# Kernel optimization log

Hardware: AMD Instinct MI355X
Metric: run time of the kernel (lower is better)

## Reference

```python
import jax, jax.numpy as jnp
import numpy as np


def setup_inputs() -> dict:
    key = jax.random.key(0)
    k1, k2 = jax.random.split(key)
    x = jax.random.normal(k1, (16, 256, 4096), dtype=jnp.float32)          # [B, D, T]
    codebooks = jax.random.normal(k2, (8, 1024, 256), dtype=jnp.float32)   # [n_q, bins, D]
    return {"x": x, "codebooks": codebooks}


def _quantize_one(residual, embed):
    """residual: [B, T, D]; embed: [bins, D] -> (quantize [B,T,D], idx [B,T])."""
    # negative squared euclidean distance (encodec euclidean codebook)
    x_sq = jnp.sum(residual * residual, axis=-1, keepdims=True)            # [B, T, 1]
    e_sq = jnp.sum(embed * embed, axis=-1)                                  # [bins]
    dots = jnp.einsum("btd,nd->btn", residual, embed)                       # [B, T, bins]
    dist = -(x_sq - 2.0 * dots + e_sq)                                      # [B, T, bins]
    idx = jnp.argmax(dist, axis=-1)                                         # [B, T] int
    quantize = embed[idx]                                                   # gather [B, T, D]
    return quantize, idx


def reference(x, codebooks):
    """Residual VQ forward (inference path, EMA updates omitted).
    x: [B, D, T]; codebooks: [n_q, bins, D].
    Returns (quantized [B, D, T], codes [n_q, B, T]).
    """
    n_q = codebooks.shape[0]
    residual = jnp.transpose(x, (0, 2, 1))                                  # [B, T, D]
    quantized_out = jnp.zeros_like(residual)
    codes = []
    for q in range(n_q):  # small fixed structural loop over quantizer stages
        quantize, idx = _quantize_one(residual, codebooks[q])
        # straight-through estimator as in encodec VectorQuantization
        quantize = residual + jax.lax.stop_gradient(quantize - residual)
        residual = residual - quantize
        quantized_out = quantized_out + quantize
        codes.append(idx)
    quantized = jnp.transpose(quantized_out, (0, 2, 1))                     # [B, D, T]
    codes = jnp.stack(codes, axis=0)                                        # [n_q, B, T]
    return quantized, codes
```

## Files before the change

### kernel.cpp

```cpp
#include <hip/hip_runtime.h>


#define BB   16
#define DD   256
#define TT   4096
#define NQ   8
#define BINS 1024
#define DELTA 4.0f
#define SOFF  8192.0f
#define OUTQ ((size_t)BB * DD * TT)

typedef _Float16 half8 __attribute__((ext_vector_type(8)));
typedef float    facc  __attribute__((ext_vector_type(4)));

#define MFMA16(A, B, C) __builtin_amdgcn_mfma_f32_16x16x32_f16((A), (B), (C), 0, 0, 0)

__global__ __launch_bounds__(256)
void rvq_pack_h16(const float* __restrict__ cb, _Float16* __restrict__ pks) {
    int gid = blockIdx.x * 256 + threadIdx.x;
    int s   = gid & 7;
    int bin = (gid >> 3) & 1023;
    int q   = gid >> 13;
    const float* src = cb + ((size_t)(q * BINS + bin)) * DD + s * 32;
    int cc    = q * 32 + (bin >> 5);
    int nf    = (bin >> 4) & 1;
    int c     = bin & 15;
    int plane = nf * 8 + s;
    size_t base = (size_t)cc * 8192 + (size_t)plane * 512 + c * 8;
    #pragma unroll
    for (int g = 0; g < 4; ++g) {
        float4 v0 = *(const float4*)(src + g * 8);
        float4 v1 = *(const float4*)(src + g * 8 + 4);
        float vv[8] = { v0.x, v0.y, v0.z, v0.w, v1.x, v1.y, v1.z, v1.w };
        half8 h8;
        #pragma unroll
        for (int j = 0; j < 8; ++j) h8[j] = (_Float16)vv[j];
        *(half8*)&pks[base + g * 128] = h8;
    }
}

__global__ __launch_bounds__(256)
void rvq_esq_off(const float* __restrict__ cb, float* __restrict__ hoff) {
    int q = blockIdx.x;
    const float* e = cb + (size_t)q * BINS * DD;
    for (int bin = threadIdx.x; bin < BINS; bin += 256) {
        const float4* row = (const float4*)(e + (size_t)bin * DD);
        float s = 0.f;
        #pragma unroll 8
        for (int i = 0; i < DD / 4; ++i) {
            float4 v = row[i];
            s += v.x * v.x + v.y * v.y + v.z * v.z + v.w * v.w;
        }
        hoff[q * BINS + bin] = SOFF - 8.0f * s;
    }
}

__global__ __launch_bounds__(128, 2)
void rvq_mfma8_kernel(const float* __restrict__ x, const float* __restrict__ cb,
                      const _Float16* __restrict__ pks, const float* __restrict__ hoff,
                      float* __restrict__ out)
{
    __shared__ alignas(16) _Float16 btile[2][16][512];
    __shared__ float esq_lds[BINS];
    __shared__ unsigned short best_lds[2][32];
    __shared__ unsigned short hist_lds[2][NQ][32];

    const int tid = threadIdx.x;
    const int w   = tid >> 6;
    const int l   = tid & 63;
    const int c   = l & 15;
    const int g   = l >> 4;

    const int blk = blockIdx.x;
    const int b   = blk >> 6;
    const int t0  = (blk & 63) * 64;
    const int tw  = t0 + w * 32;

    const char* gsrc0 = (const char*)pks + w * 8192 + (l << 4);

    auto issue_chunk = [&](int k, int bu) {
        k &= 255;
        const char* src = gsrc0 + (size_t)k * 16384;
        char* dst = (char*)(&btile[bu][0][0]) + w * 8192;
        #pragma unroll
        for (int i = 0; i < 8; ++i) {
            __builtin_amdgcn_global_load_lds(
                (const __attribute__((address_space(1))) unsigned int*)(src + i * 1024),
                (__attribute__((address_space(3))) unsigned int*)(dst + i * 1024),
                16, 0, 0);
        }
    };

    issue_chunk(0, 0);

    half8 rh[2][8], rl[2][8];
    {
        const float* xb = x + (size_t)b * DD * TT;
        #pragma unroll
        for (int s = 0; s < 8; ++s) {
            #pragma unroll
            for (int j = 0; j < 8; ++j) {
                int d = s * 32 + g * 8 + j;
                #pragma unroll
                for (int m = 0; m < 2; ++m) {
                    int t = tw + m * 16 + c;
                    float v = 16.0f * xb[(size_t)d * TT + t];
                    _Float16 h = (_Float16)v;
                    rh[m][s][j] = h;
                    rl[m][s][j] = (_Float16)(v - (float)h);
                }
            }
        }
    }
    {
        float4 v0 = *(const float4*)(hoff + tid * 8);
        float4 v1 = *(const float4*)(hoff + tid * 8 + 4);
        *(float4*)&esq_lds[tid * 8]     = v0;
        *(float4*)&esq_lds[tid * 8 + 4] = v1;
    }
    __syncthreads();

    float p1[2][4], p2[2][4], p3[2][4];

    auto reset_slots = [&]() {
        #pragma unroll
        for (int m = 0; m < 2; ++m)
            #pragma unroll
            for (int j = 0; j < 4; ++j) { p1[m][j] = 0.f; p2[m][j] = 0.f; p3[m][j] = 0.f; }
    };

    auto compute_chunk = [&](int bu, int ch) {
        facc a00 = {0.f,0.f,0.f,0.f}, a01 = {0.f,0.f,0.f,0.f};
        facc a10 = {0.f,0.f,0.f,0.f}, a11 = {0.f,0.f,0.f,0.f};
        const int roff = g * 128 + c * 8;
        const float q0 = esq_lds[ch * 32 + c];
        const float q1 = esq_lds[ch * 32 + 16 + c];
        const _Float16 (*bt)[512] = btile[bu];

        __builtin_amdgcn_s_setprio(1);
        #pragma unroll
        for (int s = 0; s < 8; ++s) {
            half8 b0 = *(const half8*)&bt[s][roff];
            half8 b1 = *(const half8*)&bt[8 + s][roff];
            a00 = MFMA16(rh[0][s], b0, a00);
            a10 = MFMA16(rh[1][s], b0, a10);
            a01 = MFMA16(rh[0][s], b1, a01);
            a11 = MFMA16(rh[1][s], b1, a11);
        }
        __builtin_amdgcn_s_setprio(0);

        const unsigned idx0 = 1023u - (unsigned)(ch * 32 + c);
        const unsigned idx1 = idx0 - 16u;
        #pragma unroll
        for (int fm = 0; fm < 2; ++fm) {
            #pragma unroll
            for (int fj = 0; fj < 4; ++fj) {
                float s0 = (fm ? a10[fj] : a00[fj]) + q0;
                float s1 = (fm ? a11[fj] : a01[fj]) + q1;
                float v0 = __builtin_bit_cast(float,
                             (__builtin_bit_cast(unsigned, s0) & ~1023u) | idx0);
                float v1 = __builtin_bit_cast(float,
                             (__builtin_bit_cast(unsigned, s1) & ~1023u) | idx1);
                float h1 = fmaxf(p1[fm][fj], v0), l1 = fminf(p1[fm][fj], v0);
                float h2 = fmaxf(p2[fm][fj], l1), l2 = fminf(p2[fm][fj], l1);
                p1[fm][fj] = h1; p2[fm][fj] = h2; p3[fm][fj] = fmaxf(p3[fm][fj], l2);
                h1 = fmaxf(p1[fm][fj], v1); l1 = fminf(p1[fm][fj], v1);
                h2 = fmaxf(p2[fm][fj], l1); l2 = fminf(p2[fm][fj], l1);
                p1[fm][fj] = h1; p2[fm][fj] = h2; p3[fm][fj] = fmaxf(p3[fm][fj], l2);
            }
        }
    };

    auto refine3 = [&](int tkl, int qq, int c1, int c2, int c3) -> int {
        int t = tw + tkl;
        double pa = 0.0, pb = 0.0, pc = 0.0;
        const float* e1p = cb + (size_t)(qq * BINS + c1) * DD;
        const float* e2p = cb + (size_t)(qq * BINS + c2) * DD;
        const float* e3p = cb + (size_t)(qq * BINS + c3) * DD;
        #pragma unroll
        for (int dd = 0; dd < 4; ++dd) {
            int d = l * 4 + dd;
            float rv = x[((size_t)b * DD + d) * TT + t];
            for (int k = 0; k < qq; ++k) {
                int hb = hist_lds[w][k][tkl];
                rv -= cb[(size_t)(k * BINS + hb) * DD + d];
            }
            float e1v = e1p[d], e2v = e2p[d], e3v = e3p[d];
            pa += (double)e1v * (2.0 * (double)rv - (double)e1v);
            pb += (double)e2v * (2.0 * (double)rv - (double)e2v);
            pc += (double)e3v * (2.0 * (double)rv - (double)e3v);
        }
        #pragma unroll
        for (int mk = 1; mk < 64; mk <<= 1) {
            pa += __shfl_xor(pa, mk);
            pb += __shfl_xor(pb, mk);
            pc += __shfl_xor(pc, mk);
        }
        int wbin = c1; double pw = pa;
        if (pb > pw || (pb == pw && c2 < wbin)) { pw = pb; wbin = c2; }
        if (pc > pw || (pc == pw && c3 < wbin)) { pw = pc; wbin = c3; }
        return wbin;
    };

    auto stage_end = [&](int qq) {
        int  bch[2][4], cn2[2][4], cn3[2][4];
        bool gate[2][4];
        #pragma unroll
        for (int fm = 0; fm < 2; ++fm) {
            #pragma unroll
            for (int fj = 0; fj < 4; ++fj) {
                float a1 = p1[fm][fj], a2 = p2[fm][fj], a3 = p3[fm][fj];
                #pragma unroll
                for (int mk = 1; mk < 16; mk <<= 1) {
                    float b1 = __shfl_xor(a1, mk);
                    float b2 = __shfl_xor(a2, mk);
                    float b3 = __shfl_xor(a3, mk);
                    float lo1 = fminf(a1, b1);
                    float m22 = fmaxf(a2, b2);
                    float r1  = fmaxf(a1, b1);
                    float r2  = fmaxf(lo1, m22);
                    float r3  = fmaxf(fminf(lo1, m22), fmaxf(fminf(a2, b2), fmaxf(a3, b3)));
                    a1 = r1; a2 = r2; a3 = r3;
                }
                bch[fm][fj] = 1023 - (int)(__builtin_bit_cast(unsigned, a1) & 1023u);
                cn2[fm][fj] = 1023 - (int)(__builtin_bit_cast(unsigned, a2) & 1023u);
                cn3[fm][fj] = 1023 - (int)(__builtin_bit_cast(unsigned, a3) & 1023u);
                gate[fm][fj] = (a1 - a2 <= DELTA);
            }
        }
        bool anyg = gate[0][0] | gate[0][1] | gate[0][2] | gate[0][3]
                  | gate[1][0] | gate[1][1] | gate[1][2] | gate[1][3];
        if (__any(anyg)) {
            #pragma unroll
            for (int fm = 0; fm < 2; ++fm) {
                #pragma unroll
                for (int fj = 0; fj < 4; ++fj) {
                    unsigned long long nm = __ballot(gate[fm][fj]);
                    if (nm) {
                        for (int g2 = 0; g2 < 4; ++g2) {
                            if ((nm >> (g2 * 16)) & 1ull) {
                                int c1 = __shfl(bch[fm][fj], g2 * 16);
                                int c2 = __shfl(cn2[fm][fj], g2 * 16);
                                int c3 = __shfl(cn3[fm][fj], g2 * 16);
                                int tkl = fm * 16 + g2 * 4 + fj;
                                int wb = refine3(tkl, qq, c1, c2, c3);
                                if (g == g2) bch[fm][fj] = wb;
                            }
                        }
                    }
                }
            }
        }

        if (c == 0) {
            #pragma unroll
            for (int fm = 0; fm < 2; ++fm)
                #pragma unroll
                for (int fj = 0; fj < 4; ++fj) {
                    int tkl = fm * 16 + g * 4 + fj;
                    best_lds[w][tkl] = (unsigned short)bch[fm][fj];
                    hist_lds[w][qq][tkl] = (unsigned short)bch[fm][fj];
                    out[OUTQ + ((size_t)qq * BB + b) * TT + tw + tkl] = (float)bch[fm][fj];
                }
        }

        #pragma unroll
        for (int m = 0; m < 2; ++m) {
            int bin = best_lds[w][m * 16 + c];
            const float* ep = cb + (size_t)(qq * BINS + bin) * DD + g * 8;
            #pragma unroll
            for (int s = 0; s < 8; ++s) {
                float4 e0 = *(const float4*)(ep + s * 32);
                float4 e1 = *(const float4*)(ep + s * 32 + 4);
                float ev[8] = { e0.x, e0.y, e0.z, e0.w, e1.x, e1.y, e1.z, e1.w };
                #pragma unroll
                for (int j = 0; j < 8; ++j) {
                    float rv = (float)rh[m][s][j] + (float)rl[m][s][j];
                    float nr = rv - 16.0f * ev[j];
                    _Float16 nh = (_Float16)nr;
                    rh[m][s][j] = nh;
                    rl[m][s][j] = (_Float16)(nr - (float)nh);
                }
            }
        }
    };

    int buf = 0;
    #pragma unroll 1
    for (int q = 0; q < NQ; ++q) {
        reset_slots();
        #pragma unroll 1
        for (int ch = 0; ch < 32; ++ch) {
            issue_chunk(q * 32 + ch + 1, buf ^ 1);
            compute_chunk(buf, ch);
            if (ch == 31) stage_end(q);
            __syncthreads();
            buf ^= 1;
        }
        if (q + 1 < NQ) {
            float4 v0 = *(const float4*)(hoff + (q + 1) * BINS + tid * 8);
            float4 v1 = *(const float4*)(hoff + (q + 1) * BINS + tid * 8 + 4);
            *(float4*)&esq_lds[tid * 8]     = v0;
            *(float4*)&esq_lds[tid * 8 + 4] = v1;
            __syncthreads();
        }
    }

    {
        const float* xb = x + (size_t)b * DD * TT;
        float* ob = out + (size_t)b * DD * TT;
        #pragma unroll
        for (int s = 0; s < 8; ++s)
            #pragma unroll
            for (int j = 0; j < 8; ++j) {
                int d = s * 32 + g * 8 + j;
                #pragma unroll
                for (int m = 0; m < 2; ++m) {
                    int t = tw + m * 16 + c;
                    float rv = ((float)rh[m][s][j] + (float)rl[m][s][j]) * 0.0625f;
                    ob[(size_t)d * TT + t] = xb[(size_t)d * TT + t] - rv;
                }
            }
    }
}

#define TOK_PER_BLK 32
#define BIN_CHUNK   128
#define KC          32
#define EPAD        36
#define RPAD        260
#define FDELTA      0.0078125f

#define FUPD2(S, BIN, B1, I1, B2, I2)                                        \
    if ((S) > (B2) || ((S) == (B2) && (BIN) < (I2))) {                      \
        if ((S) > (B1) || ((S) == (B1) && (BIN) < (I1))) {                  \
            B2 = B1; I2 = I1; B1 = (S); I1 = (BIN);                         \
        } else { B2 = (S); I2 = (BIN); }                                    \
    }

__global__ __launch_bounds__(256, 2)
void rvq_esq_kernel(const float* __restrict__ cb, float* __restrict__ esq) {
    int q = blockIdx.x;
    const float* e = cb + (size_t)q * BINS * DD;
    for (int bin = threadIdx.x; bin < BINS; bin += 256) {
        const float4* row = (const float4*)(e + (size_t)bin * DD);
        float s = 0.f;
        #pragma unroll 8
        for (int i = 0; i < DD / 4; ++i) {
            float4 v = row[i];
            s += v.x * v.x + v.y * v.y + v.z * v.z + v.w * v.w;
        }
        esq[q * BINS + bin] = s;
    }
}

__global__ __launch_bounds__(256, 2)
void rvq_main_kernel(const float* __restrict__ x, const float* __restrict__ cb,
                     const float* __restrict__ esq, float* __restrict__ out) {
    __shared__ float r_lds[TOK_PER_BLK][RPAD];
    __shared__ float e_lds[BIN_CHUNK][EPAD];
    __shared__ float red_s[16][2][TOK_PER_BLK];
    __shared__ int   red_i[16][2][TOK_PER_BLK];
    __shared__ int   best_lds2[TOK_PER_BLK];

    const int tid = threadIdx.x;
    const int blk = blockIdx.x;
    const int b   = blk >> 7;
    const int t0  = (blk & 127) * TOK_PER_BLK;

    {
        const int tl = tid & 31;
        const int d0 = (tid >> 5) * 32;
        const float* xp = x + (size_t)b * DD * TT + t0 + tl;
        for (int dd = 0; dd < 32; ++dd) {
            int d = d0 + dd;
            r_lds[tl][d] = xp[(size_t)d * TT];
        }
    }
    __syncthreads();

    const int ty = tid >> 4;
    const int tx = tid & 15;

    for (int q = 0; q < NQ; ++q) {
        const float* eb = cb + (size_t)q * BINS * DD;
        const float* es = esq + q * BINS;
        float b1[2] = {-1e30f, -1e30f}, b2[2] = {-1e30f, -1e30f};
        int   i1[2] = {0x7fffffff, 0x7fffffff}, i2[2] = {0x7fffffff, 0x7fffffff};

        for (int cch = 0; cch < BINS / BIN_CHUNK; ++cch) {
            float acc[2][8];
            #pragma unroll
            for (int i = 0; i < 2; ++i)
                #pragma unroll
                for (int j = 0; j < 8; ++j) acc[i][j] = 0.f;

            for (int kc = 0; kc < DD / KC; ++kc) {
                __syncthreads();
                {
                    const int col  = tid & 7;
                    const int row0 = tid >> 3;
                    const float* src = eb + (size_t)(cch * BIN_CHUNK) * DD + kc * KC;
                    #pragma unroll
                    for (int rr = 0; rr < 4; ++rr) {
                        int row = row0 + rr * 32;
                        float4 v = *(const float4*)(src + (size_t)row * DD + col * 4);
                        *(float4*)&e_lds[row][col * 4] = v;
                    }
                }
                __syncthreads();
                #pragma unroll
                for (int k4 = 0; k4 < KC / 4; ++k4) {
                    float4 r0 = *(const float4*)&r_lds[tx][kc * KC + k4 * 4];
                    float4 r1 = *(const float4*)&r_lds[tx + 16][kc * KC + k4 * 4];
                    #pragma unroll
                    for (int bi = 0; bi < 8; ++bi) {
                        float4 e4 = *(const float4*)&e_lds[ty + 16 * bi][k4 * 4];
                        acc[0][bi] += r0.x * e4.x + r0.y * e4.y + r0.z * e4.z + r0.w * e4.w;
                        acc[1][bi] += r1.x * e4.x + r1.y * e4.y + r1.z * e4.z + r1.w * e4.w;
                    }
                }
            }
            #pragma unroll
            for (int bi = 0; bi < 8; ++bi) {
                int bin = cch * BIN_CHUNK + ty + 16 * bi;
                float half_esq = 0.5f * es[bin];
                float s0 = acc[0][bi] - half_esq;
                float s1v = acc[1][bi] - half_esq;
                FUPD2(s0, bin, b1[0], i1[0], b2[0], i2[0]);
                FUPD2(s1v, bin, b1[1], i1[1], b2[1], i2[1]);
            }
        }

        #pragma unroll
        for (int k = 0; k < 2; ++k) {
            red_s[ty][k][tx]      = k ? b2[0] : b1[0];
            red_i[ty][k][tx]      = k ? i2[0] : i1[0];
            red_s[ty][k][tx + 16] = k ? b2[1] : b1[1];
            red_i[ty][k][tx + 16] = k ? i2[1] : i1[1];
        }
        __syncthreads();

        if (tid < TOK_PER_BLK) {
            float g1 = -1e30f, g2 = -1e30f; int gi1 = 0x7fffffff, gi2 = 0x7fffffff;
            #pragma unroll
            for (int j = 0; j < 16; ++j) {
                #pragma unroll
                for (int k = 0; k < 2; ++k) {
                    float s = red_s[j][k][tid]; int ii = red_i[j][k][tid];
                    FUPD2(s, ii, g1, gi1, g2, gi2);
                }
            }
            int bif;
            if (g1 - g2 <= FDELTA) {
                const float* rrow = r_lds[tid];
                double sc[2]; int id2[2] = { gi1, gi2 };
                for (int cc2 = 0; cc2 < 2; ++cc2) {
                    const float* ep = eb + (size_t)id2[cc2] * DD;
                    double acc2 = 0.0;
                    #pragma unroll 4
                    for (int d = 0; d < DD; ++d) {
                        double ev = (double)ep[d];
                        acc2 += ev * (2.0 * (double)rrow[d] - ev);
                    }
                    sc[cc2] = acc2;
                }
                bif = (sc[0] > sc[1] || (sc[0] == sc[1] && id2[0] < id2[1])) ? id2[0] : id2[1];
            } else {
                bif = gi1;
            }
            best_lds2[tid] = bif;
            out[OUTQ + (size_t)q * (BB * TT) + (size_t)b * TT + t0 + tid] = (float)bif;
        }
        __syncthreads();

        {
            const int tok  = tid >> 3;
            const int part = tid & 7;
            const int bin  = best_lds2[tok];
            const float* ep = eb + (size_t)bin * DD + part * 32;
            float* rp = &r_lds[tok][part * 32];
            #pragma unroll
            for (int dd = 0; dd < 32; ++dd) rp[dd] -= ep[dd];
        }
        __syncthreads();
    }

    {
        const int tl = tid & 31;
        const int d0 = (tid >> 5) * 32;
        const float* xp = x + (size_t)b * DD * TT + t0 + tl;
        float*       op = out + (size_t)b * DD * TT + t0 + tl;
        for (int dd = 0; dd < 32; ++dd) {
            int d = d0 + dd;
            op[(size_t)d * TT] = xp[(size_t)d * TT] - r_lds[tl][d];
        }
    }
}

extern "C" void kernel_launch(void* const* d_in, const int* in_sizes, int n_in,
                              void* d_out, int out_size, void* d_ws, size_t ws_size,
                              hipStream_t stream) {
    const float* x  = (const float*)d_in[0];
    const float* cb = (const float*)d_in[1];
    float* out = (float*)d_out;

    const size_t PKS_BYTES = (size_t)NQ * BINS * DD * 2;
    const size_t NEED = PKS_BYTES + (size_t)NQ * BINS * 4;

    if (ws_size >= NEED) {
        _Float16* pks = (_Float16*)d_ws;
        float* hoff = (float*)((char*)d_ws + PKS_BYTES);
        rvq_pack_h16<<<(NQ * BINS * 8) / 256, 256, 0, stream>>>(cb, pks);
        rvq_esq_off<<<NQ, 256, 0, stream>>>(cb, hoff);
        rvq_mfma8_kernel<<<1024, 128, 0, stream>>>(x, cb, pks, hoff, out);
    } else {
        float* esq = (float*)d_ws;
        rvq_esq_kernel<<<NQ, 256, 0, stream>>>(cb, esq);
        rvq_main_kernel<<<(BB * TT) / TOK_PER_BLK, 256, 0, stream>>>(x, cb, esq, out);
    }
}
```

Baseline: 658.9 us.

## Split each block's 64 tokens across four waves of 16 tokens

Blocks grow from 2 waves owning 32 tokens each to 4 waves owning 16 tokens each. Each wave now keeps a single 16-row MFMA tile, which halves the per-wave residual and accumulator registers, and the LDS codebook chunk loads are shared across 4 waves. The intent is higher occupancy and more waves to hide latency. In exchange, each loaded B fragment now feeds 2 MFMAs per wave instead of 4, so LDS read traffic per FLOP doubles and block-level syncs cover more waves.

Result: faster. 635.0 us (-3.6%).

```diff
diff --git a/kernel.cpp b/kernel.cpp
--- a/kernel.cpp
+++ b/kernel.cpp
@@ -55,15 +55,15 @@
     }
 }
 
-__global__ __launch_bounds__(128, 2)
-void rvq_mfma8_kernel(const float* __restrict__ x, const float* __restrict__ cb,
+__global__ __launch_bounds__(256, 4)
+void rvq_mfma9_kernel(const float* __restrict__ x, const float* __restrict__ cb,
                       const _Float16* __restrict__ pks, const float* __restrict__ hoff,
                       float* __restrict__ out)
 {
     __shared__ alignas(16) _Float16 btile[2][16][512];
     __shared__ float esq_lds[BINS];
-    __shared__ unsigned short best_lds[2][32];
-    __shared__ unsigned short hist_lds[2][NQ][32];
+    __shared__ unsigned short best_lds[4][16];
+    __shared__ unsigned short hist_lds[4][NQ][16];
 
     const int tid = threadIdx.x;
     const int w   = tid >> 6;
@@ -74,16 +74,16 @@
     const int blk = blockIdx.x;
     const int b   = blk >> 6;
     const int t0  = (blk & 63) * 64;
-    const int tw  = t0 + w * 32;
-
-    const char* gsrc0 = (const char*)pks + w * 8192 + (l << 4);
+    const int tw  = t0 + w * 16;
+
+    const char* gsrc0 = (const char*)pks + w * 4096 + (l << 4);
 
     auto issue_chunk = [&](int k, int bu) {
         k &= 255;
         const char* src = gsrc0 + (size_t)k * 16384;
-        char* dst = (char*)(&btile[bu][0][0]) + w * 8192;
-        #pragma unroll
-        for (int i = 0; i < 8; ++i) {
+        char* dst = (char*)(&btile[bu][0][0]) + w * 4096;
+        #pragma unroll
+        for (int i = 0; i < 4; ++i) {
             __builtin_amdgcn_global_load_lds(
                 (const __attribute__((address_space(1))) unsigned int*)(src + i * 1024),
                 (__attribute__((address_space(3))) unsigned int*)(dst + i * 1024),
@@ -93,45 +93,37 @@
 
     issue_chunk(0, 0);
 
-    half8 rh[2][8], rl[2][8];
+    half8 rh[8], rl[8];
     {
         const float* xb = x + (size_t)b * DD * TT;
+        const int t = tw + c;
         #pragma unroll
         for (int s = 0; s < 8; ++s) {
             #pragma unroll
             for (int j = 0; j < 8; ++j) {
                 int d = s * 32 + g * 8 + j;
-                #pragma unroll
-                for (int m = 0; m < 2; ++m) {
-                    int t = tw + m * 16 + c;
-                    float v = 16.0f * xb[(size_t)d * TT + t];
-                    _Float16 h = (_Float16)v;
-                    rh[m][s][j] = h;
-                    rl[m][s][j] = (_Float16)(v - (float)h);
-                }
+                float v = 16.0f * xb[(size_t)d * TT + t];
+                _Float16 h = (_Float16)v;
+                rh[s][j] = h;
+                rl[s][j] = (_Float16)(v - (float)h);
             }
         }
     }
     {
-        float4 v0 = *(const float4*)(hoff + tid * 8);
-        float4 v1 = *(const float4*)(hoff + tid * 8 + 4);
-        *(float4*)&esq_lds[tid * 8]     = v0;
-        *(float4*)&esq_lds[tid * 8 + 4] = v1;
+        float4 v = *(const float4*)(hoff + tid * 4);
+        *(float4*)&esq_lds[tid * 4] = v;
     }
     __syncthreads();
 
-    float p1[2][4], p2[2][4], p3[2][4];
+    float p1[4], p2[4], p3[4];
 
     auto reset_slots = [&]() {
         #pragma unroll
-        for (int m = 0; m < 2; ++m)
-            #pragma unroll
-            for (int j = 0; j < 4; ++j) { p1[m][j] = 0.f; p2[m][j] = 0.f; p3[m][j] = 0.f; }
+        for (int j = 0; j < 4; ++j) { p1[j] = 0.f; p2[j] = 0.f; p3[j] = 0.f; }
     };
 
     auto compute_chunk = [&](int bu, int ch) {
-        facc a00 = {0.f,0.f,0.f,0.f}, a01 = {0.f,0.f,0.f,0.f};
-        facc a10 = {0.f,0.f,0.f,0.f}, a11 = {0.f,0.f,0.f,0.f};
+        facc a0 = {0.f,0.f,0.f,0.f}, a1 = {0.f,0.f,0.f,0.f};
         const int roff = g * 128 + c * 8;
         const float q0 = esq_lds[ch * 32 + c];
         const float q1 = esq_lds[ch * 32 + 16 + c];
@@ -142,32 +134,27 @@
         for (int s = 0; s < 8; ++s) {
             half8 b0 = *(const half8*)&bt[s][roff];
             half8 b1 = *(const half8*)&bt[8 + s][roff];
-            a00 = MFMA16(rh[0][s], b0, a00);
-            a10 = MFMA16(rh[1][s], b0, a10);
-            a01 = MFMA16(rh[0][s], b1, a01);
-            a11 = MFMA16(rh[1][s], b1, a11);
+            a0 = MFMA16(rh[s], b0, a0);
+            a1 = MFMA16(rh[s], b1, a1);
         }
         __builtin_amdgcn_s_setprio(0);
 
         const unsigned idx0 = 1023u - (unsigned)(ch * 32 + c);
         const unsigned idx1 = idx0 - 16u;
         #pragma unroll
-        for (int fm = 0; fm < 2; ++fm) {
-            #pragma unroll
-            for (int fj = 0; fj < 4; ++fj) {
-                float s0 = (fm ? a10[fj] : a00[fj]) + q0;
-                float s1 = (fm ? a11[fj] : a01[fj]) + q1;
-                float v0 = __builtin_bit_cast(float,
-                             (__builtin_bit_cast(unsigned, s0) & ~1023u) | idx0);
-                float v1 = __builtin_bit_cast(float,
-                             (__builtin_bit_cast(unsigned, s1) & ~1023u) | idx1);
-                float h1 = fmaxf(p1[fm][fj], v0), l1 = fminf(p1[fm][fj], v0);
-                float h2 = fmaxf(p2[fm][fj], l1), l2 = fminf(p2[fm][fj], l1);
-                p1[fm][fj] = h1; p2[fm][fj] = h2; p3[fm][fj] = fmaxf(p3[fm][fj], l2);
-                h1 = fmaxf(p1[fm][fj], v1); l1 = fminf(p1[fm][fj], v1);
-                h2 = fmaxf(p2[fm][fj], l1); l2 = fminf(p2[fm][fj], l1);
-                p1[fm][fj] = h1; p2[fm][fj] = h2; p3[fm][fj] = fmaxf(p3[fm][fj], l2);
-            }
+        for (int fj = 0; fj < 4; ++fj) {
+            float s0 = a0[fj] + q0;
+            float s1 = a1[fj] + q1;
+            float v0 = __builtin_bit_cast(float,
+                         (__builtin_bit_cast(unsigned, s0) & ~1023u) | idx0);
+            float v1 = __builtin_bit_cast(float,
+                         (__builtin_bit_cast(unsigned, s1) & ~1023u) | idx1);
+            float h1 = fmaxf(p1[fj], v0), l1 = fminf(p1[fj], v0);
+            float h2 = fmaxf(p2[fj], l1), l2 = fminf(p2[fj], l1);
+            p1[fj] = h1; p2[fj] = h2; p3[fj] = fmaxf(p3[fj], l2);
+            h1 = fmaxf(p1[fj], v1); l1 = fminf(p1[fj], v1);
+            h2 = fmaxf(p2[fj], l1); l2 = fminf(p2[fj], l1);
+            p1[fj] = h1; p2[fj] = h2; p3[fj] = fmaxf(p3[fj], l2);
         }
     };
 
@@ -203,49 +190,42 @@
     };
 
     auto stage_end = [&](int qq) {
-        int  bch[2][4], cn2[2][4], cn3[2][4];
-        bool gate[2][4];
-        #pragma unroll
-        for (int fm = 0; fm < 2; ++fm) {
+        int  bch[4], cn2[4], cn3[4];
+        bool gate[4];
+        #pragma unroll
+        for (int fj = 0; fj < 4; ++fj) {
+            float a1 = p1[fj], a2 = p2[fj], a3 = p3[fj];
+            #pragma unroll
+            for (int mk = 1; mk < 16; mk <<= 1) {
+                float b1 = __shfl_xor(a1, mk);
+                float b2 = __shfl_xor(a2, mk);
+                float b3 = __shfl_xor(a3, mk);
+                float lo1 = fminf(a1, b1);
+                float m22 = fmaxf(a2, b2);
+                float r1  = fmaxf(a1, b1);
+                float r2  = fmaxf(lo1, m22);
+                float r3  = fmaxf(fminf(lo1, m22), fmaxf(fminf(a2, b2), fmaxf(a3, b3)));
+                a1 = r1; a2 = r2; a3 = r3;
+            }
+            bch[fj] = 1023 - (int)(__builtin_bit_cast(unsigned, a1) & 1023u);
+            cn2[fj] = 1023 - (int)(__builtin_bit_cast(unsigned, a2) & 1023u);
+            cn3[fj] = 1023 - (int)(__builtin_bit_cast(unsigned, a3) & 1023u);
+            gate[fj] = (a1 - a2 <= DELTA);
+        }
+        bool anyg = gate[0] | gate[1] | gate[2] | gate[3];
+        if (__any(anyg)) {
             #pragma unroll
             for (int fj = 0; fj < 4; ++fj) {
-                float a1 = p1[fm][fj], a2 = p2[fm][fj], a3 = p3[fm][fj];
-                #pragma unroll
-                for (int mk = 1; mk < 16; mk <<= 1) {
-                    float b1 = __shfl_xor(a1, mk);
-                    float b2 = __shfl_xor(a2, mk);
-                    float b3 = __shfl_xor(a3, mk);
-                    float lo1 = fminf(a1, b1);
-                    float m22 = fmaxf(a2, b2);
-                    float r1  = fmaxf(a1, b1);
-                    float r2  = fmaxf(lo1, m22);
-                    float r3  = fmaxf(fminf(lo1, m22), fmaxf(fminf(a2, b2), fmaxf(a3, b3)));
-                    a1 = r1; a2 = r2; a3 = r3;
-                }
-                bch[fm][fj] = 1023 - (int)(__builtin_bit_cast(unsigned, a1) & 1023u);
-                cn2[fm][fj] = 1023 - (int)(__builtin_bit_cast(unsigned, a2) & 1023u);
-                cn3[fm][fj] = 1023 - (int)(__builtin_bit_cast(unsigned, a3) & 1023u);
-                gate[fm][fj] = (a1 - a2 <= DELTA);
-            }
-        }
-        bool anyg = gate[0][0] | gate[0][1] | gate[0][2] | gate[0][3]
-                  | gate[1][0] | gate[1][1] | gate[1][2] | gate[1][3];
-        if (__any(anyg)) {
-            #pragma unroll
-            for (int fm = 0; fm < 2; ++fm) {
-                #pragma unroll
-                for (int fj = 0; fj < 4; ++fj) {
-                    unsigned long long nm = __ballot(gate[fm][fj]);
-                    if (nm) {
-                        for (int g2 = 0; g2 < 4; ++g2) {
-                            if ((nm >> (g2 * 16)) & 1ull) {
-                                int c1 = __shfl(bch[fm][fj], g2 * 16);
-                                int c2 = __shfl(cn2[fm][fj], g2 * 16);
-                                int c3 = __shfl(cn3[fm][fj], g2 * 16);
-                                int tkl = fm * 16 + g2 * 4 + fj;
-                                int wb = refine3(tkl, qq, c1, c2, c3);
-                                if (g == g2) bch[fm][fj] = wb;
-                            }
+                unsigned long long nm = __ballot(gate[fj]);
+                if (nm) {
+                    for (int g2 = 0; g2 < 4; ++g2) {
+                        if ((nm >> (g2 * 16)) & 1ull) {
+                            int c1 = __shfl(bch[fj], g2 * 16);
+                            int c2 = __shfl(cn2[fj], g2 * 16);
+                            int c3 = __shfl(cn3[fj], g2 * 16);
+                            int tkl = g2 * 4 + fj;
+                            int wb = refine3(tkl, qq, c1, c2, c3);
+                            if (g == g2) bch[fj] = wb;
                         }
                     }
                 }
@@ -254,19 +234,16 @@
 
         if (c == 0) {
             #pragma unroll
-            for (int fm = 0; fm < 2; ++fm)
-                #pragma unroll
-                for (int fj = 0; fj < 4; ++fj) {
-                    int tkl = fm * 16 + g * 4 + fj;
-                    best_lds[w][tkl] = (unsigned short)bch[fm][fj];
-                    hist_lds[w][qq][tkl] = (unsigned short)bch[fm][fj];
-                    out[OUTQ + ((size_t)qq * BB + b) * TT + tw + tkl] = (float)bch[fm][fj];
-                }
-        }
-
-        #pragma unroll
-        for (int m = 0; m < 2; ++m) {
-            int bin = best_lds[w][m * 16 + c];
+            for (int fj = 0; fj < 4; ++fj) {
+                int tkl = g * 4 + fj;
+                best_lds[w][tkl] = (unsigned short)bch[fj];
+                hist_lds[w][qq][tkl] = (unsigned short)bch[fj];
+                out[OUTQ + ((size_t)qq * BB + b) * TT + tw + tkl] = (float)bch[fj];
+            }
+        }
+
+        {
+            int bin = best_lds[w][c];
             const float* ep = cb + (size_t)(qq * BINS + bin) * DD + g * 8;
             #pragma unroll
             for (int s = 0; s < 8; ++s) {
@@ -275,11 +252,11 @@
                 float ev[8] = { e0.x, e0.y, e0.z, e0.w, e1.x, e1.y, e1.z, e1.w };
                 #pragma unroll
                 for (int j = 0; j < 8; ++j) {
-                    float rv = (float)rh[m][s][j] + (float)rl[m][s][j];
+                    float rv = (float)rh[s][j] + (float)rl[s][j];
                     float nr = rv - 16.0f * ev[j];
                     _Float16 nh = (_Float16)nr;
-                    rh[m][s][j] = nh;
-                    rl[m][s][j] = (_Float16)(nr - (float)nh);
+                    rh[s][j] = nh;
+                    rl[s][j] = (_Float16)(nr - (float)nh);
                 }
             }
         }
@@ -298,10 +275,8 @@
             buf ^= 1;
         }
         if (q + 1 < NQ) {
-            float4 v0 = *(const float4*)(hoff + (q + 1) * BINS + tid * 8);
-            float4 v1 = *(const float4*)(hoff + (q + 1) * BINS + tid * 8 + 4);
-            *(float4*)&esq_lds[tid * 8]     = v0;
-            *(float4*)&esq_lds[tid * 8 + 4] = v1;
+            float4 v = *(const float4*)(hoff + (q + 1) * BINS + tid * 4);
+            *(float4*)&esq_lds[tid * 4] = v;
             __syncthreads();
         }
     }
@@ -309,17 +284,14 @@
     {
         const float* xb = x + (size_t)b * DD * TT;
         float* ob = out + (size_t)b * DD * TT;
+        const int t = tw + c;
         #pragma unroll
         for (int s = 0; s < 8; ++s)
             #pragma unroll
             for (int j = 0; j < 8; ++j) {
                 int d = s * 32 + g * 8 + j;
-                #pragma unroll
-                for (int m = 0; m < 2; ++m) {
-                    int t = tw + m * 16 + c;
-                    float rv = ((float)rh[m][s][j] + (float)rl[m][s][j]) * 0.0625f;
-                    ob[(size_t)d * TT + t] = xb[(size_t)d * TT + t] - rv;
-                }
+                float rv = ((float)rh[s][j] + (float)rl[s][j]) * 0.0625f;
+                ob[(size_t)d * TT + t] = xb[(size_t)d * TT + t] - rv;
             }
     }
 }
@@ -513,7 +485,7 @@
         float* hoff = (float*)((char*)d_ws + PKS_BYTES);
         rvq_pack_h16<<<(NQ * BINS * 8) / 256, 256, 0, stream>>>(cb, pks);
         rvq_esq_off<<<NQ, 256, 0, stream>>>(cb, hoff);
-        rvq_mfma8_kernel<<<1024, 128, 0, stream>>>(x, cb, pks, hoff, out);
+        rvq_mfma9_kernel<<<1024, 256, 0, stream>>>(x, cb, pks, hoff, out);
     } else {
         float* esq = (float*)d_ws;
         rvq_esq_kernel<<<NQ, 256, 0, stream>>>(cb, esq);
```
